# Kernel tuning notes

Measured on AMD Instinct MI355X. Metric: run time of the kernel, lower is better.

Reference implementation:

```python
import jax, jax.numpy as jnp
import numpy as np

B, N, E, FIN, H, D = 256, 1024, 8192, 8, 4, 5
HD = H * D            # GATv2: 4 heads * 5 dim, concat -> 20
OBS = N               # flattened obs length
AOUT = 64             # action_space_output_dim (aggregator output)
HID = 256             # hidden_size
NOUT = 64             # num_outputs (logits)
NEG = 0.2             # GATv2 leaky_relu negative slope
EPS = 1e-5            # batchnorm eps


def setup_inputs() -> dict:
    key = jax.random.key(0)
    ks = jax.random.split(key, 16)
    def lin(k, i, o):
        return (jax.random.normal(k, (i, o), jnp.float32) / np.sqrt(i)).astype(jnp.float32)
    return {
        "x": jax.random.normal(ks[0], (B, N, FIN), jnp.float32),
        "obs": jax.random.normal(ks[1], (B, OBS), jnp.float32),
        "edge_index": jax.random.randint(ks[2], (2, E), 0, N),
        # GATv2 layer 0 (in=FIN) and layer 1 (in=HD)
        "Wl0": lin(ks[3], FIN, HD), "Wr0": lin(ks[4], FIN, HD),
        "att0": (jax.random.normal(ks[5], (H, D), jnp.float32) * 0.1), "b0": jnp.zeros((HD,), jnp.float32),
        "Wl1": lin(ks[6], HD, HD), "Wr1": lin(ks[7], HD, HD),
        "att1": (jax.random.normal(ks[8], (H, D), jnp.float32) * 0.1), "b1": jnp.zeros((HD,), jnp.float32),
        # BatchNorm params per layer (over feature dim)
        "g0": jnp.ones((HD,), jnp.float32), "be0": jnp.zeros((HD,), jnp.float32),
        "g1": jnp.ones((HD,), jnp.float32), "be1": jnp.zeros((HD,), jnp.float32),
        # aggregator linear (mean pool -> action-space dim)
        "Wagg": lin(ks[9], HD, AOUT), "bagg": jnp.zeros((AOUT,), jnp.float32),
        # logits MLP: cat(agg, obs) -> HID -> HID//2 -> NOUT (tanh activations)
        "W1": lin(ks[10], AOUT + OBS, HID), "bh1": jnp.zeros((HID,), jnp.float32),
        "W2": lin(ks[11], HID, HID // 2), "bh2": jnp.zeros((HID // 2,), jnp.float32),
        "Wout": lin(ks[12], HID // 2, NOUT), "bout": jnp.zeros((NOUT,), jnp.float32),
    }


def _gatv2_single(x, src, dst, Wl, Wr, att, bias):
    # x: [N, Fin]; src/dst: [Es] (with self loops)
    xl = (x @ Wl).reshape(N, H, D)
    xr = (x @ Wr).reshape(N, H, D)
    m = jax.nn.leaky_relu(xl[src] + xr[dst], NEG)        # [Es, H, D]
    e = jnp.einsum('ehd,hd->eh', m, att)                 # [Es, H]
    emax = jax.ops.segment_max(e, dst, num_segments=N)   # every node has a self loop
    p = jnp.exp(e - emax[dst])
    s = jax.ops.segment_sum(p, dst, num_segments=N)
    alpha = p / s[dst]                                   # softmax over incoming edges
    out = jax.ops.segment_sum(alpha[:, :, None] * xl[src], dst, num_segments=N)
    return out.reshape(N, HD) + bias


def _bn(x, g, b):
    # training-mode batchnorm over all (batch, node) positions, per feature
    mu = x.mean(axis=(0, 1))
    var = x.var(axis=(0, 1))
    return (x - mu) * jax.lax.rsqrt(var + EPS) * g + b


def reference(x, obs, edge_index, Wl0, Wr0, att0, b0, Wl1, Wr1, att1, b1,
              g0, be0, g1, be1, Wagg, bagg, W1, bh1, W2, bh2, Wout, bout):
    loops = jnp.arange(N)
    src = jnp.concatenate([edge_index[0], loops])
    dst = jnp.concatenate([edge_index[1], loops])
    layer = lambda xb, Wl, Wr, att, bias: jax.vmap(
        lambda xn: _gatv2_single(xn, src, dst, Wl, Wr, att, bias))(xb)
    h = layer(x, Wl0, Wr0, att0, b0)       # [B, N, HD]
    h = _bn(h, g0, be0)
    h = layer(h, Wl1, Wr1, att1, b1)
    h = _bn(h, g1, be1)
    agg = h.mean(axis=1) @ Wagg + bagg     # mean graph pooling -> [B, AOUT]
    f = jnp.concatenate([agg, obs], axis=1)
    f = jnp.tanh(f @ W1 + bh1)
    f = jnp.tanh(f @ W2 + bh2)
    return f @ Wout + bout                 # logits [B, NOUT]
```

## Files before the change

kernel.cpp:

```cpp
#include <hip/hip_runtime.h>
#include <hip/hip_bf16.h>
#include <math.h>

typedef unsigned short u16;
typedef __attribute__((ext_vector_type(8))) short short8;
typedef __attribute__((ext_vector_type(4))) float floatx4;

constexpr int kN   = 1024;
constexpr int kB   = 256;
constexpr int kE   = 8192;
constexpr int kHD  = 20;
constexpr float kEps = 1e-5f;

static __device__ __forceinline__ float u16_bf16_to_f32(u16 v) {
  return __uint_as_float(((unsigned)v) << 16);
}
static __device__ __forceinline__ void unpack2(unsigned u, float& a, float& b) {
  a = __uint_as_float(u << 16);
  b = __uint_as_float(u & 0xffff0000u);
}
static __device__ __forceinline__ u16 f2bf(float f) {
  __hip_bfloat16 h = __float2bfloat16(f);
  return *reinterpret_cast<u16*>(&h);
}
static __device__ __forceinline__ unsigned pack_bf16(float a, float b) {
  return (unsigned)f2bf(a) | ((unsigned)f2bf(b) << 16);
}

__global__ __launch_bounds__(64) void detect_kernel(const unsigned* __restrict__ x,
                                                    int* __restrict__ flag) {
  unsigned w = x[threadIdx.x];
  unsigned e = (w >> 7) & 0xFFu;
  bool plaus = (e >= 114u && e <= 136u);
  unsigned long long b = __ballot(plaus);
  if (threadIdx.x == 0) *flag = (__popcll(b) >= 32) ? 1 : 0;
}

struct SmallConv {
  const void* src[17];
  float* dst[17];
  int n[17];
};

__global__ __launch_bounds__(256) void small_conv_kernel(SmallConv a, const int* __restrict__ flag) {
  int t = blockIdx.x;
  int n = a.n[t];
  float* d = a.dst[t];
  if (*flag) {
    const u16* s = (const u16*)a.src[t];
    for (int i = threadIdx.x; i < n; i += 256) d[i] = u16_bf16_to_f32(s[i]);
  } else {
    const float* s = (const float*)a.src[t];
    for (int i = threadIdx.x; i < n; i += 256) d[i] = s[i];
  }
}

__global__ __launch_bounds__(256) void convert_x_kernel(const void* __restrict__ src,
                                                        float* __restrict__ x_f,
                                                        const int* __restrict__ flag) {
  int rid = blockIdx.x * 256 + threadIdx.x;
  int b = rid >> 10, n = rid & 1023;
  float v[8];
  if (*flag) {
    uint4 r = *((const uint4*)((const u16*)src + (size_t)rid * 8));
    unpack2(r.x, v[0], v[1]); unpack2(r.y, v[2], v[3]);
    unpack2(r.z, v[4], v[5]); unpack2(r.w, v[6], v[7]);
  } else {
    const float4* s = (const float4*)((const float*)src + (size_t)rid * 8);
    float4 r0 = s[0], r1 = s[1];
    v[0] = r0.x; v[1] = r0.y; v[2] = r0.z; v[3] = r0.w;
    v[4] = r1.x; v[5] = r1.y; v[6] = r1.z; v[7] = r1.w;
  }
  float* d = x_f + ((size_t)n * kB + b) * 8;
  ((float4*)d)[0] = make_float4(v[0], v[1], v[2], v[3]);
  ((float4*)d)[1] = make_float4(v[4], v[5], v[6], v[7]);
}

static __device__ __forceinline__ void repack_one(const void* src, u16* dst, int c, int N, int srcbf) {
  int n = c % N;
  int t2 = c / N;
  int q = t2 & 3, kb = t2 >> 2;
  int k0 = kb * 32 + q * 8;
  u16 w[8];
  if (srcbf) {
    const u16* s = (const u16*)src;
#pragma unroll
    for (int j = 0; j < 8; j++) w[j] = s[(size_t)(k0 + j) * N + n];
  } else {
    const float* s = (const float*)src;
#pragma unroll
    for (int j = 0; j < 8; j++) w[j] = f2bf(s[(size_t)(k0 + j) * N + n]);
  }
  uint4 out;
  out.x = (unsigned)w[0] | ((unsigned)w[1] << 16);
  out.y = (unsigned)w[2] | ((unsigned)w[3] << 16);
  out.z = (unsigned)w[4] | ((unsigned)w[5] << 16);
  out.w = (unsigned)w[6] | ((unsigned)w[7] << 16);
  *((uint4*)(dst + (size_t)c * 8)) = out;
}

__global__ __launch_bounds__(256) void repack_kernel(const void* __restrict__ W1,
                                                     const void* __restrict__ W2,
                                                     const void* __restrict__ Wout,
                                                     u16* __restrict__ W1p,
                                                     u16* __restrict__ W2p,
                                                     u16* __restrict__ Woutp,
                                                     const int* __restrict__ flag) {
  int c = blockIdx.x * 256 + threadIdx.x;
  int srcbf = *flag;
  if (c < 34816) repack_one(W1, W1p, c, 256, srcbf);
  else if (c < 34816 + 4096) repack_one(W2, W2p, c - 34816, 128, srcbf);
  else if (c < 34816 + 4096 + 1024) repack_one(Wout, Woutp, c - 34816 - 4096, 64, srcbf);
}

__global__ __launch_bounds__(1024) void build_csr_kernel(const int* __restrict__ ei,
                                                         int* __restrict__ csr_off,
                                                         int* __restrict__ csr_src) {
  __shared__ int cnt[kN];
  __shared__ int tmp[kN];
  __shared__ int cur[kN];
  int t = threadIdx.x;
  cnt[t] = 0;
  __syncthreads();
  for (int e = t; e < kE; e += 1024) atomicAdd(&cnt[ei[kE + e]], 1);
  __syncthreads();
  int deg = cnt[t] + 1;
  tmp[t] = deg;
  __syncthreads();
  for (int o = 1; o < kN; o <<= 1) {
    int add = (t >= o) ? tmp[t - o] : 0;
    __syncthreads();
    tmp[t] += add;
    __syncthreads();
  }
  int excl = tmp[t] - deg;
  csr_off[t] = excl;
  cur[t] = excl;
  if (t == kN - 1) csr_off[kN] = tmp[t];
  __syncthreads();
  for (int e = t; e < kE; e += 1024) {
    int s = ei[e], d2 = ei[kE + e];
    int pos = atomicAdd(&cur[d2], 1);
    csr_src[pos] = s;
  }
  int pos = atomicAdd(&cur[t], 1);
  csr_src[pos] = t;
}

__global__ __launch_bounds__(256) void lin0_kernel(const float* __restrict__ x,
                                                   const float* __restrict__ Wl,
                                                   const float* __restrict__ Wr,
                                                   u16* __restrict__ xlb,
                                                   u16* __restrict__ xrb) {
  __shared__ float wl[8 * kHD], wr[8 * kHD];
  int t = threadIdx.x;
  if (t < 8 * kHD) { wl[t] = Wl[t]; wr[t] = Wr[t]; }
  __syncthreads();
  int n = blockIdx.x, b = t;
  const float4* xp = (const float4*)(x + ((size_t)n * kB + b) * 8);
  float xi[8];
  {
    float4 v0 = xp[0], v1 = xp[1];
    xi[0] = v0.x; xi[1] = v0.y; xi[2] = v0.z; xi[3] = v0.w;
    xi[4] = v1.x; xi[5] = v1.y; xi[6] = v1.z; xi[7] = v1.w;
  }
  float ol[kHD], orr[kHD];
#pragma unroll
  for (int f = 0; f < kHD; f++) {
    float al = 0.f, ar = 0.f;
#pragma unroll
    for (int i = 0; i < 8; i++) {
      al = fmaf(xi[i], wl[i * kHD + f], al);
      ar = fmaf(xi[i], wr[i * kHD + f], ar);
    }
    ol[f] = al; orr[f] = ar;
  }
  uint2* pl = (uint2*)(xlb + ((size_t)n * kB + b) * kHD);
  uint2* pr = (uint2*)(xrb + ((size_t)n * kB + b) * kHD);
#pragma unroll
  for (int k = 0; k < 5; k++) {
    pl[k] = make_uint2(pack_bf16(ol[4 * k], ol[4 * k + 1]), pack_bf16(ol[4 * k + 2], ol[4 * k + 3]));
    pr[k] = make_uint2(pack_bf16(orr[4 * k], orr[4 * k + 1]), pack_bf16(orr[4 * k + 2], orr[4 * k + 3]));
  }
}

__global__ __launch_bounds__(256) void lin1_kernel(const u16* __restrict__ hb,
                                                   const float* __restrict__ Wlp,
                                                   const float* __restrict__ Wrp,
                                                   const float* __restrict__ blp,
                                                   const float* __restrict__ brp,
                                                   u16* __restrict__ xlb,
                                                   u16* __restrict__ xrb) {
  __shared__ float wl[kHD * kHD], wr[kHD * kHD], sbl[kHD], sbr[kHD];
  int t = threadIdx.x;
  for (int idx = t; idx < kHD * kHD; idx += 256) { wl[idx] = Wlp[idx]; wr[idx] = Wrp[idx]; }
  if (t < kHD) { sbl[t] = blp[t]; sbr[t] = brp[t]; }
  __syncthreads();
  int n = blockIdx.x, b = t;
  float hv[kHD];
  {
    const uint2* p = (const uint2*)(hb + ((size_t)n * kB + b) * kHD);
#pragma unroll
    for (int k = 0; k < 5; k++) {
      uint2 v = p[k];
      unpack2(v.x, hv[4 * k], hv[4 * k + 1]);
      unpack2(v.y, hv[4 * k + 2], hv[4 * k + 3]);
    }
  }
  float ol[kHD], orr[kHD];
#pragma unroll
  for (int j = 0; j < kHD; j++) {
    float al = sbl[j], ar = sbr[j];
#pragma unroll
    for (int f = 0; f < kHD; f++) {
      al = fmaf(hv[f], wl[f * kHD + j], al);
      ar = fmaf(hv[f], wr[f * kHD + j], ar);
    }
    ol[j] = al; orr[j] = ar;
  }
  uint2* pl = (uint2*)(xlb + ((size_t)n * kB + b) * kHD);
  uint2* pr = (uint2*)(xrb + ((size_t)n * kB + b) * kHD);
#pragma unroll
  for (int k = 0; k < 5; k++) {
    pl[k] = make_uint2(pack_bf16(ol[4 * k], ol[4 * k + 1]), pack_bf16(ol[4 * k + 2], ol[4 * k + 3]));
    pr[k] = make_uint2(pack_bf16(orr[4 * k], orr[4 * k + 1]), pack_bf16(orr[4 * k + 2], orr[4 * k + 3]));
  }
}

__global__ __launch_bounds__(128) void attn_kernel(const u16* __restrict__ xlb,
                                                   const u16* __restrict__ xrb,
                                                   const int* __restrict__ csr_off,
                                                   const int* __restrict__ csr_src,
                                                   const float* __restrict__ att,
                                                   const float* __restrict__ bias,
                                                   u16* __restrict__ hout,
                                                   float* __restrict__ sums) {
  __shared__ float satt[kHD], sbias[kHD];
  __shared__ float red[2][2 * kHD];
  int t = threadIdx.x;
  if (t < kHD) { satt[t] = att[t]; sbias[t] = bias[t]; }
  __syncthreads();
  int n = blockIdx.x >> 1;
  int b = ((blockIdx.x & 1) << 7) | t;

  float xrv[kHD];
  {
    const uint2* p = (const uint2*)(xrb + ((size_t)n * kB + b) * kHD);
#pragma unroll
    for (int k = 0; k < 5; k++) {
      uint2 v = p[k];
      unpack2(v.x, xrv[4 * k], xrv[4 * k + 1]);
      unpack2(v.y, xrv[4 * k + 2], xrv[4 * k + 3]);
    }
  }
  float s[4] = {0.f, 0.f, 0.f, 0.f};
  float acc[kHD];
#pragma unroll
  for (int f = 0; f < kHD; f++) acc[f] = 0.f;

  int beg = csr_off[n], end = csr_off[n + 1];
  uint2 r[5];
  {
    const uint2* p = (const uint2*)(xlb + ((size_t)csr_src[beg] * kB + b) * kHD);
#pragma unroll
    for (int k = 0; k < 5; k++) r[k] = p[k];
  }
  for (int idx = beg; idx < end; idx++) {
    float xs[kHD];
#pragma unroll
    for (int k = 0; k < 5; k++) {
      unpack2(r[k].x, xs[4 * k], xs[4 * k + 1]);
      unpack2(r[k].y, xs[4 * k + 2], xs[4 * k + 3]);
    }
    if (idx + 1 < end) {
      const uint2* p = (const uint2*)(xlb + ((size_t)csr_src[idx + 1] * kB + b) * kHD);
#pragma unroll
      for (int k = 0; k < 5; k++) r[k] = p[k];
    }
#pragma unroll
    for (int hh = 0; hh < 4; hh++) {
      float e = 0.f;
#pragma unroll
      for (int d = 0; d < 5; d++) {
        int f = hh * 5 + d;
        float v = xs[f] + xrv[f];
        v = fmaxf(v, 0.2f * v);
        e = fmaf(v, satt[f], e);
      }
      float p = __expf(e);
      s[hh] += p;
#pragma unroll
      for (int d = 0; d < 5; d++) {
        int f = hh * 5 + d;
        acc[f] = fmaf(p, xs[f], acc[f]);
      }
    }
  }
  float hv[kHD];
#pragma unroll
  for (int hh = 0; hh < 4; hh++) {
    float inv = 1.f / s[hh];
#pragma unroll
    for (int d = 0; d < 5; d++) {
      int f = hh * 5 + d;
      hv[f] = fmaf(acc[f], inv, sbias[f]);
    }
  }
  {
    uint2* ph = (uint2*)(hout + ((size_t)n * kB + b) * kHD);
#pragma unroll
    for (int k = 0; k < 5; k++)
      ph[k] = make_uint2(pack_bf16(hv[4 * k], hv[4 * k + 1]), pack_bf16(hv[4 * k + 2], hv[4 * k + 3]));
  }
  int lane = t & 63, wv = t >> 6;
#pragma unroll
  for (int f = 0; f < kHD; f++) {
    float a = hv[f], q = hv[f] * hv[f];
    for (int o = 32; o > 0; o >>= 1) { a += __shfl_down(a, o); q += __shfl_down(q, o); }
    if (lane == 0) { red[wv][f] = a; red[wv][kHD + f] = q; }
  }
  __syncthreads();
  if (t < 2 * kHD) atomicAdd(&sums[(blockIdx.x & 7) * 2 * kHD + t], red[0][t] + red[1][t]);
}

__global__ __launch_bounds__(256) void fold_kernel(const float* __restrict__ sums,
                                                   const float* __restrict__ g,
                                                   const float* __restrict__ be,
                                                   const float* __restrict__ Wl1,
                                                   const float* __restrict__ Wr1,
                                                   float* __restrict__ Wlp, float* __restrict__ Wrp,
                                                   float* __restrict__ blp, float* __restrict__ brp) {
  __shared__ float a[kHD], c[kHD];
  __shared__ float tot[2 * kHD];
  int t = threadIdx.x;
  if (t < 2 * kHD) {
    float v = 0.f;
    for (int k = 0; k < 8; k++) v += sums[k * 2 * kHD + t];
    tot[t] = v;
  }
  __syncthreads();
  if (t < kHD) {
    const float inv = 1.0f / (float)(kN * kB);
    float mu = tot[t] * inv;
    float var = tot[kHD + t] * inv - mu * mu;
    float av = g[t] * rsqrtf(var + kEps);
    a[t] = av;
    c[t] = be[t] - mu * av;
  }
  __syncthreads();
  for (int idx = t; idx < kHD * kHD; idx += 256) {
    int f = idx / kHD;
    Wlp[idx] = a[f] * Wl1[idx];
    Wrp[idx] = a[f] * Wr1[idx];
  }
  if (t < kHD) {
    float sl = 0.f, sr = 0.f;
    for (int f = 0; f < kHD; f++) {
      sl += c[f] * Wl1[f * kHD + t];
      sr += c[f] * Wr1[f * kHD + t];
    }
    blp[t] = sl;
    brp[t] = sr;
  }
}

__global__ __launch_bounds__(256) void pool_fin_kernel(const u16* __restrict__ hb,
                                                       const float* __restrict__ sums,
                                                       const float* __restrict__ g1,
                                                       const float* __restrict__ be1,
                                                       const float* __restrict__ Wagg,
                                                       const float* __restrict__ bagg,
                                                       const void* __restrict__ obsraw,
                                                       const int* __restrict__ flag,
                                                       u16* __restrict__ finb) {
  int b = blockIdx.x, t = threadIdx.x;
  float acc[kHD];
#pragma unroll
  for (int f = 0; f < kHD; f++) acc[f] = 0.f;
  for (int n = t; n < kN; n += 256) {
    const uint2* p = (const uint2*)(hb + ((size_t)n * kB + b) * kHD);
#pragma unroll
    for (int k = 0; k < 5; k++) {
      uint2 v = p[k];
      float a0, a1, a2, a3;
      unpack2(v.x, a0, a1); unpack2(v.y, a2, a3);
      acc[4 * k] += a0; acc[4 * k + 1] += a1; acc[4 * k + 2] += a2; acc[4 * k + 3] += a3;
    }
  }
  __shared__ float red[4][kHD];
  __shared__ float tot[2 * kHD], pv[kHD];
#pragma unroll
  for (int f = 0; f < kHD; f++) {
    float v = acc[f];
    for (int o = 32; o > 0; o >>= 1) v += __shfl_down(v, o);
    if ((t & 63) == 0) red[t >> 6][f] = v;
  }
  if (t < 2 * kHD) {
    float v = 0.f;
    for (int k = 0; k < 8; k++) v += sums[k * 2 * kHD + t];
    tot[t] = v;
  }
  __syncthreads();
  if (t < kHD) {
    const float inv = 1.0f / (float)(kN * kB);
    float mu = tot[t] * inv;
    float var = tot[kHD + t] * inv - mu * mu;
    float a1 = g1[t] * rsqrtf(var + kEps);
    float c1 = be1[t] - mu * a1;
    float pool = (red[0][t] + red[1][t] + red[2][t] + red[3][t]) * (1.0f / kN);
    pv[t] = pool * a1 + c1;
  }
  __syncthreads();
  if (t < 64) {
    float agg = bagg[t];
#pragma unroll
    for (int f = 0; f < kHD; f++) agg = fmaf(pv[f], Wagg[f * 64 + t], agg);
    finb[(size_t)b * 1088 + t] = f2bf(agg);
  }
  if (t < 128) {
    uint4* dst = (uint4*)(finb + (size_t)b * 1088 + 64 + t * 8);
    if (*flag) {
      *dst = *((const uint4*)((const u16*)obsraw + (size_t)b * 1024 + t * 8));
    } else {
      const float4* s = (const float4*)((const float*)obsraw + (size_t)b * 1024 + t * 8);
      float4 r0 = s[0], r1 = s[1];
      uint4 o;
      o.x = pack_bf16(r0.x, r0.y); o.y = pack_bf16(r0.z, r0.w);
      o.z = pack_bf16(r1.x, r1.y); o.w = pack_bf16(r1.z, r1.w);
      *dst = o;
    }
  }
}

__global__ __launch_bounds__(256) void mlp1_kernel(const u16* __restrict__ finb,
                                                   const u16* __restrict__ W1p,
                                                   const float* __restrict__ bh1,
                                                   u16* __restrict__ h1b) {
  int tid = threadIdx.x;
  int wave = tid >> 6, lane = tid & 63;
  int tile = blockIdx.x * 4 + wave;
  int m0 = (tile >> 4) << 4, n0 = (tile & 15) << 4;
  int lo = lane & 15, quad = lane >> 4;
  floatx4 acc = {0.f, 0.f, 0.f, 0.f};
  const u16* ap = finb + (size_t)(m0 + lo) * 1088 + quad * 8;
  const u16* bp = W1p + ((size_t)quad * 256 + n0 + lo) * 8;
  for (int kb = 0; kb < 34; kb++) {
    short8 a = *(const short8*)ap; ap += 32;
    short8 bfr = *(const short8*)bp; bp += 4 * 256 * 8;
    acc = __builtin_amdgcn_mfma_f32_16x16x32_bf16(a, bfr, acc, 0, 0, 0);
  }
  float bias = bh1[n0 + lo];
  u16* op = h1b + (size_t)(m0 + quad * 4) * 256 + n0 + lo;
#pragma unroll
  for (int r = 0; r < 4; r++) op[r * 256] = f2bf(tanhf(acc[r] + bias));
}

__global__ __launch_bounds__(256) void mlp23_kernel(const u16* __restrict__ h1b,
                                                    const u16* __restrict__ W2p,
                                                    const u16* __restrict__ Woutp,
                                                    const float* __restrict__ bh2,
                                                    const float* __restrict__ bout,
                                                    const int* __restrict__ flag,
                                                    void* __restrict__ outv) {
  __shared__ __align__(16) u16 h2s[16][128];
  int tid = threadIdx.x;
  int wave = tid >> 6, lane = tid & 63;
  int lo = lane & 15, quad = lane >> 4;
  int m0 = blockIdx.x * 16;
#pragma unroll
  for (int i = 0; i < 2; i++) {
    int n0 = (wave * 2 + i) * 16;
    floatx4 acc = {0.f, 0.f, 0.f, 0.f};
    const u16* ap = h1b + (size_t)(m0 + lo) * 256 + quad * 8;
    const u16* bp = W2p + ((size_t)quad * 128 + n0 + lo) * 8;
    for (int kb = 0; kb < 8; kb++) {
      short8 a = *(const short8*)ap; ap += 32;
      short8 bfr = *(const short8*)bp; bp += 4 * 128 * 8;
      acc = __builtin_amdgcn_mfma_f32_16x16x32_bf16(a, bfr, acc, 0, 0, 0);
    }
    float bias = bh2[n0 + lo];
#pragma unroll
    for (int r = 0; r < 4; r++) h2s[quad * 4 + r][n0 + lo] = f2bf(tanhf(acc[r] + bias));
  }
  __syncthreads();
  {
    int n0 = wave * 16;
    floatx4 acc = {0.f, 0.f, 0.f, 0.f};
    const u16* bp = Woutp + ((size_t)quad * 64 + n0 + lo) * 8;
    for (int kb = 0; kb < 4; kb++) {
      short8 a = *(const short8*)(&h2s[lo][kb * 32 + quad * 8]);
      short8 bfr = *(const short8*)bp; bp += 4 * 64 * 8;
      acc = __builtin_amdgcn_mfma_f32_16x16x32_bf16(a, bfr, acc, 0, 0, 0);
    }
    float bias = bout[n0 + lo];
    if (*flag) {
      __hip_bfloat16* o = (__hip_bfloat16*)outv;
#pragma unroll
      for (int r = 0; r < 4; r++)
        o[(size_t)(m0 + quad * 4 + r) * 64 + n0 + lo] = __float2bfloat16(acc[r] + bias);
    } else {
      float* o = (float*)outv;
#pragma unroll
      for (int r = 0; r < 4; r++)
        o[(size_t)(m0 + quad * 4 + r) * 64 + n0 + lo] = acc[r] + bias;
    }
  }
}

extern "C" void kernel_launch(void* const* d_in, const int* in_sizes, int n_in,
                              void* d_out, int out_size, void* d_ws, size_t ws_size,
                              hipStream_t stream) {
  const int* ei = (const int*)d_in[2];
  char* ws = (char*)d_ws;

  float* sums0   = (float*)(ws + 0);
  float* sums1   = (float*)(ws + 1280);
  int*   flag    = (int*)(ws + 2560);
  int*   csr_off = (int*)(ws + 2816);
  int*   csr_src = (int*)(ws + 7168);
  float* Wlp     = (float*)(ws + 44288);
  float* Wrp     = (float*)(ws + 45888);
  float* blp     = (float*)(ws + 47488);
  float* brp     = (float*)(ws + 47568);
  float* convf   = (float*)(ws + 47872);
  u16*   W1p     = (u16*)(ws + 60416);
  u16*   W2p     = (u16*)(ws + 617472);
  u16*   Woutp   = (u16*)(ws + 683008);
  u16*   finb    = (u16*)(ws + 699392);
  u16*   h1b     = (u16*)(ws + 1256448);
  float* x_f     = (float*)(ws + 1387520);
  u16*   xlb     = (u16*)(ws + 9776128);
  u16*   xrb     = (u16*)(ws + 20261888);
  u16*   hb      = (u16*)(ws + 30747648);

  const int s_din[17] = {3, 4, 5, 6, 7, 8, 9, 10, 11, 12, 13, 14, 15, 16, 18, 20, 22};
  const int s_n[17]   = {160, 160, 20, 20, 400, 400, 20, 20, 20, 20, 20, 20, 1280, 64, 256, 128, 64};
  SmallConv sc;
  float* fptr[17];
  {
    size_t co = 0;
    for (int i = 0; i < 17; i++) {
      sc.src[i] = d_in[s_din[i]];
      sc.dst[i] = convf + co;
      sc.n[i] = s_n[i];
      fptr[i] = convf + co;
      co += (size_t)s_n[i];
    }
  }
  float* Wl0_f = fptr[0],  *Wr0_f = fptr[1],  *att0_f = fptr[2], *b0_f = fptr[3];
  float* Wl1_f = fptr[4],  *Wr1_f = fptr[5],  *att1_f = fptr[6], *b1_f = fptr[7];
  float* g0_f = fptr[8],   *be0_f = fptr[9],  *g1_f = fptr[10],  *be1_f = fptr[11];
  float* Wagg_f = fptr[12], *bagg_f = fptr[13], *bh1_f = fptr[14], *bh2_f = fptr[15];
  float* bout_f = fptr[16];

  hipMemsetAsync(ws, 0, 2560, stream);
  detect_kernel<<<1, 64, 0, stream>>>((const unsigned*)d_in[0], flag);
  small_conv_kernel<<<17, 256, 0, stream>>>(sc, flag);
  convert_x_kernel<<<1024, 256, 0, stream>>>(d_in[0], x_f, flag);
  repack_kernel<<<156, 256, 0, stream>>>(d_in[17], d_in[19], d_in[21], W1p, W2p, Woutp, flag);
  build_csr_kernel<<<1, 1024, 0, stream>>>(ei, csr_off, csr_src);

  lin0_kernel<<<kN, 256, 0, stream>>>(x_f, Wl0_f, Wr0_f, xlb, xrb);
  attn_kernel<<<2 * kN, 128, 0, stream>>>(xlb, xrb, csr_off, csr_src, att0_f, b0_f, hb, sums0);
  fold_kernel<<<1, 256, 0, stream>>>(sums0, g0_f, be0_f, Wl1_f, Wr1_f, Wlp, Wrp, blp, brp);
  lin1_kernel<<<kN, 256, 0, stream>>>(hb, Wlp, Wrp, blp, brp, xlb, xrb);
  attn_kernel<<<2 * kN, 128, 0, stream>>>(xlb, xrb, csr_off, csr_src, att1_f, b1_f, hb, sums1);
  pool_fin_kernel<<<kB, 256, 0, stream>>>(hb, sums1, g1_f, be1_f, Wagg_f, bagg_f,
                                          d_in[1], flag, finb);
  mlp1_kernel<<<64, 256, 0, stream>>>(finb, W1p, bh1_f, h1b);
  mlp23_kernel<<<16, 256, 0, stream>>>(h1b, W2p, Woutp, bh2_f, bout_f, flag, d_out);
}
```

Measured before the change: 234.5 us.

## Fuse setup kernels and fold BN into lin1, reducing launch count

Merges the memset, dtype detection, small-parameter conversion, x conversion, weight repack, CSR build and layer-0 linear into one multi-role setup kernel. The x transpose now happens inside lin0, so the fp32 staging buffer goes away. The BatchNorm fold is merged into lin1, and every kernel recomputes the dtype flag and converts its parameters inline instead of reading pre-converted copies. The aim is to remove about seven launches and an extra pass over x. The cost is redundant per-block flag detection and parameter conversion, plus a serial CSR block that now shares its launch with heavy work.

```diff
diff --git a/kernel.cpp b/kernel.cpp
--- a/kernel.cpp
+++ b/kernel.cpp
@@ -27,56 +27,20 @@
   return (unsigned)f2bf(a) | ((unsigned)f2bf(b) << 16);
 }
 
-__global__ __launch_bounds__(64) void detect_kernel(const unsigned* __restrict__ x,
-                                                    int* __restrict__ flag) {
-  unsigned w = x[threadIdx.x];
+static __device__ __forceinline__ int detect_flag(const unsigned* __restrict__ x) {
+  unsigned w = x[threadIdx.x & 63];
   unsigned e = (w >> 7) & 0xFFu;
   bool plaus = (e >= 114u && e <= 136u);
   unsigned long long b = __ballot(plaus);
-  if (threadIdx.x == 0) *flag = (__popcll(b) >= 32) ? 1 : 0;
-}
-
-struct SmallConv {
-  const void* src[17];
-  float* dst[17];
-  int n[17];
-};
-
-__global__ __launch_bounds__(256) void small_conv_kernel(SmallConv a, const int* __restrict__ flag) {
-  int t = blockIdx.x;
-  int n = a.n[t];
-  float* d = a.dst[t];
-  if (*flag) {
-    const u16* s = (const u16*)a.src[t];
-    for (int i = threadIdx.x; i < n; i += 256) d[i] = u16_bf16_to_f32(s[i]);
-  } else {
-    const float* s = (const float*)a.src[t];
-    for (int i = threadIdx.x; i < n; i += 256) d[i] = s[i];
-  }
-}
-
-__global__ __launch_bounds__(256) void convert_x_kernel(const void* __restrict__ src,
-                                                        float* __restrict__ x_f,
-                                                        const int* __restrict__ flag) {
-  int rid = blockIdx.x * 256 + threadIdx.x;
-  int b = rid >> 10, n = rid & 1023;
-  float v[8];
-  if (*flag) {
-    uint4 r = *((const uint4*)((const u16*)src + (size_t)rid * 8));
-    unpack2(r.x, v[0], v[1]); unpack2(r.y, v[2], v[3]);
-    unpack2(r.z, v[4], v[5]); unpack2(r.w, v[6], v[7]);
-  } else {
-    const float4* s = (const float4*)((const float*)src + (size_t)rid * 8);
-    float4 r0 = s[0], r1 = s[1];
-    v[0] = r0.x; v[1] = r0.y; v[2] = r0.z; v[3] = r0.w;
-    v[4] = r1.x; v[5] = r1.y; v[6] = r1.z; v[7] = r1.w;
-  }
-  float* d = x_f + ((size_t)n * kB + b) * 8;
-  ((float4*)d)[0] = make_float4(v[0], v[1], v[2], v[3]);
-  ((float4*)d)[1] = make_float4(v[4], v[5], v[6], v[7]);
-}
-
-static __device__ __forceinline__ void repack_one(const void* src, u16* dst, int c, int N, int srcbf) {
+  return (__popcll(b) >= 32) ? 1 : 0;
+}
+static __device__ __forceinline__ float ldconv(const void* __restrict__ p, int i, int flag) {
+  return flag ? u16_bf16_to_f32(((const u16*)p)[i]) : ((const float*)p)[i];
+}
+
+static __device__ __forceinline__ void repack_one(const void* __restrict__ src,
+                                                  u16* __restrict__ dst,
+                                                  int c, int N, int srcbf) {
   int n = c % N;
   int t2 = c / N;
   int q = t2 & 3, kb = t2 >> 2;
@@ -99,131 +63,89 @@
   *((uint4*)(dst + (size_t)c * 8)) = out;
 }
 
-__global__ __launch_bounds__(256) void repack_kernel(const void* __restrict__ W1,
-                                                     const void* __restrict__ W2,
-                                                     const void* __restrict__ Wout,
-                                                     u16* __restrict__ W1p,
-                                                     u16* __restrict__ W2p,
-                                                     u16* __restrict__ Woutp,
-                                                     const int* __restrict__ flag) {
-  int c = blockIdx.x * 256 + threadIdx.x;
-  int srcbf = *flag;
-  if (c < 34816) repack_one(W1, W1p, c, 256, srcbf);
-  else if (c < 34816 + 4096) repack_one(W2, W2p, c - 34816, 128, srcbf);
-  else if (c < 34816 + 4096 + 1024) repack_one(Wout, Woutp, c - 34816 - 4096, 64, srcbf);
-}
-
-__global__ __launch_bounds__(1024) void build_csr_kernel(const int* __restrict__ ei,
-                                                         int* __restrict__ csr_off,
-                                                         int* __restrict__ csr_src) {
-  __shared__ int cnt[kN];
-  __shared__ int tmp[kN];
-  __shared__ int cur[kN];
+__global__ __launch_bounds__(1024) void setup_kernel(
+    const unsigned* __restrict__ xdet,
+    const void* __restrict__ xin,
+    const int* __restrict__ ei,
+    const void* __restrict__ Wl0, const void* __restrict__ Wr0,
+    const void* __restrict__ W1, const void* __restrict__ W2, const void* __restrict__ Wout,
+    int* __restrict__ csr_off, int* __restrict__ csr_src,
+    float* __restrict__ sums,
+    u16* __restrict__ W1p, u16* __restrict__ W2p, u16* __restrict__ Woutp,
+    u16* __restrict__ xlb, u16* __restrict__ xrb) {
+  int bid = blockIdx.x;
   int t = threadIdx.x;
-  cnt[t] = 0;
-  __syncthreads();
-  for (int e = t; e < kE; e += 1024) atomicAdd(&cnt[ei[kE + e]], 1);
-  __syncthreads();
-  int deg = cnt[t] + 1;
-  tmp[t] = deg;
-  __syncthreads();
-  for (int o = 1; o < kN; o <<= 1) {
-    int add = (t >= o) ? tmp[t - o] : 0;
+  if (bid == 0) {
+    __shared__ int cnt[kN];
+    __shared__ int tmp[kN];
+    __shared__ int cur[kN];
+    cnt[t] = 0;
     __syncthreads();
-    tmp[t] += add;
+    for (int e = t; e < kE; e += 1024) atomicAdd(&cnt[ei[kE + e]], 1);
     __syncthreads();
-  }
-  int excl = tmp[t] - deg;
-  csr_off[t] = excl;
-  cur[t] = excl;
-  if (t == kN - 1) csr_off[kN] = tmp[t];
-  __syncthreads();
-  for (int e = t; e < kE; e += 1024) {
-    int s = ei[e], d2 = ei[kE + e];
-    int pos = atomicAdd(&cur[d2], 1);
-    csr_src[pos] = s;
-  }
-  int pos = atomicAdd(&cur[t], 1);
-  csr_src[pos] = t;
-}
-
-__global__ __launch_bounds__(256) void lin0_kernel(const float* __restrict__ x,
-                                                   const float* __restrict__ Wl,
-                                                   const float* __restrict__ Wr,
-                                                   u16* __restrict__ xlb,
-                                                   u16* __restrict__ xrb) {
-  __shared__ float wl[8 * kHD], wr[8 * kHD];
-  int t = threadIdx.x;
-  if (t < 8 * kHD) { wl[t] = Wl[t]; wr[t] = Wr[t]; }
-  __syncthreads();
-  int n = blockIdx.x, b = t;
-  const float4* xp = (const float4*)(x + ((size_t)n * kB + b) * 8);
-  float xi[8];
-  {
-    float4 v0 = xp[0], v1 = xp[1];
-    xi[0] = v0.x; xi[1] = v0.y; xi[2] = v0.z; xi[3] = v0.w;
-    xi[4] = v1.x; xi[5] = v1.y; xi[6] = v1.z; xi[7] = v1.w;
-  }
-  float ol[kHD], orr[kHD];
-#pragma unroll
-  for (int f = 0; f < kHD; f++) {
-    float al = 0.f, ar = 0.f;
-#pragma unroll
-    for (int i = 0; i < 8; i++) {
-      al = fmaf(xi[i], wl[i * kHD + f], al);
-      ar = fmaf(xi[i], wr[i * kHD + f], ar);
-    }
-    ol[f] = al; orr[f] = ar;
-  }
-  uint2* pl = (uint2*)(xlb + ((size_t)n * kB + b) * kHD);
-  uint2* pr = (uint2*)(xrb + ((size_t)n * kB + b) * kHD);
-#pragma unroll
-  for (int k = 0; k < 5; k++) {
-    pl[k] = make_uint2(pack_bf16(ol[4 * k], ol[4 * k + 1]), pack_bf16(ol[4 * k + 2], ol[4 * k + 3]));
-    pr[k] = make_uint2(pack_bf16(orr[4 * k], orr[4 * k + 1]), pack_bf16(orr[4 * k + 2], orr[4 * k + 3]));
-  }
-}
-
-__global__ __launch_bounds__(256) void lin1_kernel(const u16* __restrict__ hb,
-                                                   const float* __restrict__ Wlp,
-                                                   const float* __restrict__ Wrp,
-                                                   const float* __restrict__ blp,
-                                                   const float* __restrict__ brp,
-                                                   u16* __restrict__ xlb,
-                                                   u16* __restrict__ xrb) {
-  __shared__ float wl[kHD * kHD], wr[kHD * kHD], sbl[kHD], sbr[kHD];
-  int t = threadIdx.x;
-  for (int idx = t; idx < kHD * kHD; idx += 256) { wl[idx] = Wlp[idx]; wr[idx] = Wrp[idx]; }
-  if (t < kHD) { sbl[t] = blp[t]; sbr[t] = brp[t]; }
-  __syncthreads();
-  int n = blockIdx.x, b = t;
-  float hv[kHD];
-  {
-    const uint2* p = (const uint2*)(hb + ((size_t)n * kB + b) * kHD);
+    int deg = cnt[t] + 1;
+    tmp[t] = deg;
+    __syncthreads();
+    for (int o = 1; o < kN; o <<= 1) {
+      int add = (t >= o) ? tmp[t - o] : 0;
+      __syncthreads();
+      tmp[t] += add;
+      __syncthreads();
+    }
+    int excl = tmp[t] - deg;
+    csr_off[t] = excl;
+    cur[t] = excl;
+    if (t == kN - 1) csr_off[kN] = tmp[t];
+    __syncthreads();
+    for (int e = t; e < kE; e += 1024) {
+      int s = ei[e], d2 = ei[kE + e];
+      int pos = atomicAdd(&cur[d2], 1);
+      csr_src[pos] = s;
+    }
+    int pos = atomicAdd(&cur[t], 1);
+    csr_src[pos] = t;
+    if (t < 640) sums[t] = 0.f;
+  } else if (bid <= 39) {
+    int flag = detect_flag(xdet);
+    int c = (bid - 1) * 1024 + t;
+    if (c < 34816) repack_one(W1, W1p, c, 256, flag);
+    else if (c < 38912) repack_one(W2, W2p, c - 34816, 128, flag);
+    else repack_one(Wout, Woutp, c - 38912, 64, flag);
+  } else {
+    int flag = detect_flag(xdet);
+    __shared__ float wl[8 * kHD], wr[8 * kHD];
+    if (t < 8 * kHD) { wl[t] = ldconv(Wl0, t, flag); wr[t] = ldconv(Wr0, t, flag); }
+    __syncthreads();
+    int n = (bid - 40) * 4 + (t >> 8), b = t & 255;
+    float xi[8];
+    if (flag) {
+      uint4 r = *((const uint4*)((const u16*)xin + ((size_t)b * kN + n) * 8));
+      unpack2(r.x, xi[0], xi[1]); unpack2(r.y, xi[2], xi[3]);
+      unpack2(r.z, xi[4], xi[5]); unpack2(r.w, xi[6], xi[7]);
+    } else {
+      const float4* s = (const float4*)((const float*)xin + ((size_t)b * kN + n) * 8);
+      float4 v0 = s[0], v1 = s[1];
+      xi[0] = v0.x; xi[1] = v0.y; xi[2] = v0.z; xi[3] = v0.w;
+      xi[4] = v1.x; xi[5] = v1.y; xi[6] = v1.z; xi[7] = v1.w;
+    }
+    float ol[kHD], orr[kHD];
+#pragma unroll
+    for (int f = 0; f < kHD; f++) {
+      float al = 0.f, ar = 0.f;
+#pragma unroll
+      for (int i = 0; i < 8; i++) {
+        al = fmaf(xi[i], wl[i * kHD + f], al);
+        ar = fmaf(xi[i], wr[i * kHD + f], ar);
+      }
+      ol[f] = al; orr[f] = ar;
+    }
+    uint2* pl = (uint2*)(xlb + ((size_t)n * kB + b) * kHD);
+    uint2* pr = (uint2*)(xrb + ((size_t)n * kB + b) * kHD);
 #pragma unroll
     for (int k = 0; k < 5; k++) {
-      uint2 v = p[k];
-      unpack2(v.x, hv[4 * k], hv[4 * k + 1]);
-      unpack2(v.y, hv[4 * k + 2], hv[4 * k + 3]);
-    }
-  }
-  float ol[kHD], orr[kHD];
-#pragma unroll
-  for (int j = 0; j < kHD; j++) {
-    float al = sbl[j], ar = sbr[j];
-#pragma unroll
-    for (int f = 0; f < kHD; f++) {
-      al = fmaf(hv[f], wl[f * kHD + j], al);
-      ar = fmaf(hv[f], wr[f * kHD + j], ar);
-    }
-    ol[j] = al; orr[j] = ar;
-  }
-  uint2* pl = (uint2*)(xlb + ((size_t)n * kB + b) * kHD);
-  uint2* pr = (uint2*)(xrb + ((size_t)n * kB + b) * kHD);
-#pragma unroll
-  for (int k = 0; k < 5; k++) {
-    pl[k] = make_uint2(pack_bf16(ol[4 * k], ol[4 * k + 1]), pack_bf16(ol[4 * k + 2], ol[4 * k + 3]));
-    pr[k] = make_uint2(pack_bf16(orr[4 * k], orr[4 * k + 1]), pack_bf16(orr[4 * k + 2], orr[4 * k + 3]));
+      pl[k] = make_uint2(pack_bf16(ol[4 * k], ol[4 * k + 1]), pack_bf16(ol[4 * k + 2], ol[4 * k + 3]));
+      pr[k] = make_uint2(pack_bf16(orr[4 * k], orr[4 * k + 1]), pack_bf16(orr[4 * k + 2], orr[4 * k + 3]));
+    }
   }
 }
 
@@ -231,14 +153,16 @@
                                                    const u16* __restrict__ xrb,
                                                    const int* __restrict__ csr_off,
                                                    const int* __restrict__ csr_src,
-                                                   const float* __restrict__ att,
-                                                   const float* __restrict__ bias,
+                                                   const void* __restrict__ attraw,
+                                                   const void* __restrict__ braw,
+                                                   const unsigned* __restrict__ xdet,
                                                    u16* __restrict__ hout,
                                                    float* __restrict__ sums) {
   __shared__ float satt[kHD], sbias[kHD];
   __shared__ float red[2][2 * kHD];
+  int flag = detect_flag(xdet);
   int t = threadIdx.x;
-  if (t < kHD) { satt[t] = att[t]; sbias[t] = bias[t]; }
+  if (t < kHD) { satt[t] = ldconv(attraw, t, flag); sbias[t] = ldconv(braw, t, flag); }
   __syncthreads();
   int n = blockIdx.x >> 1;
   int b = ((blockIdx.x & 1) << 7) | t;
@@ -323,19 +247,22 @@
   if (t < 2 * kHD) atomicAdd(&sums[(blockIdx.x & 7) * 2 * kHD + t], red[0][t] + red[1][t]);
 }
 
-__global__ __launch_bounds__(256) void fold_kernel(const float* __restrict__ sums,
-                                                   const float* __restrict__ g,
-                                                   const float* __restrict__ be,
-                                                   const float* __restrict__ Wl1,
-                                                   const float* __restrict__ Wr1,
-                                                   float* __restrict__ Wlp, float* __restrict__ Wrp,
-                                                   float* __restrict__ blp, float* __restrict__ brp) {
-  __shared__ float a[kHD], c[kHD];
-  __shared__ float tot[2 * kHD];
+__global__ __launch_bounds__(256) void lin1_kernel(const u16* __restrict__ hb,
+                                                   const float* __restrict__ sums0,
+                                                   const void* __restrict__ g0,
+                                                   const void* __restrict__ be0,
+                                                   const void* __restrict__ Wl1,
+                                                   const void* __restrict__ Wr1,
+                                                   const unsigned* __restrict__ xdet,
+                                                   u16* __restrict__ xlb,
+                                                   u16* __restrict__ xrb) {
+  __shared__ float wl[kHD * kHD], wr[kHD * kHD], sbl[kHD], sbr[kHD];
+  __shared__ float sa[kHD], sc[kHD], tot[2 * kHD];
+  int flag = detect_flag(xdet);
   int t = threadIdx.x;
   if (t < 2 * kHD) {
     float v = 0.f;
-    for (int k = 0; k < 8; k++) v += sums[k * 2 * kHD + t];
+    for (int k = 0; k < 8; k++) v += sums0[k * 2 * kHD + t];
     tot[t] = v;
   }
   __syncthreads();
@@ -343,36 +270,67 @@
     const float inv = 1.0f / (float)(kN * kB);
     float mu = tot[t] * inv;
     float var = tot[kHD + t] * inv - mu * mu;
-    float av = g[t] * rsqrtf(var + kEps);
-    a[t] = av;
-    c[t] = be[t] - mu * av;
+    float av = ldconv(g0, t, flag) * rsqrtf(var + kEps);
+    sa[t] = av;
+    sc[t] = ldconv(be0, t, flag) - mu * av;
   }
   __syncthreads();
   for (int idx = t; idx < kHD * kHD; idx += 256) {
     int f = idx / kHD;
-    Wlp[idx] = a[f] * Wl1[idx];
-    Wrp[idx] = a[f] * Wr1[idx];
+    wl[idx] = sa[f] * ldconv(Wl1, idx, flag);
+    wr[idx] = sa[f] * ldconv(Wr1, idx, flag);
   }
   if (t < kHD) {
     float sl = 0.f, sr = 0.f;
     for (int f = 0; f < kHD; f++) {
-      sl += c[f] * Wl1[f * kHD + t];
-      sr += c[f] * Wr1[f * kHD + t];
-    }
-    blp[t] = sl;
-    brp[t] = sr;
+      sl += sc[f] * ldconv(Wl1, f * kHD + t, flag);
+      sr += sc[f] * ldconv(Wr1, f * kHD + t, flag);
+    }
+    sbl[t] = sl;
+    sbr[t] = sr;
+  }
+  __syncthreads();
+  int n = blockIdx.x, b = t;
+  float hv[kHD];
+  {
+    const uint2* p = (const uint2*)(hb + ((size_t)n * kB + b) * kHD);
+#pragma unroll
+    for (int k = 0; k < 5; k++) {
+      uint2 v = p[k];
+      unpack2(v.x, hv[4 * k], hv[4 * k + 1]);
+      unpack2(v.y, hv[4 * k + 2], hv[4 * k + 3]);
+    }
+  }
+  float ol[kHD], orr[kHD];
+#pragma unroll
+  for (int j = 0; j < kHD; j++) {
+    float al = sbl[j], ar = sbr[j];
+#pragma unroll
+    for (int f = 0; f < kHD; f++) {
+      al = fmaf(hv[f], wl[f * kHD + j], al);
+      ar = fmaf(hv[f], wr[f * kHD + j], ar);
+    }
+    ol[j] = al; orr[j] = ar;
+  }
+  uint2* pl = (uint2*)(xlb + ((size_t)n * kB + b) * kHD);
+  uint2* pr = (uint2*)(xrb + ((size_t)n * kB + b) * kHD);
+#pragma unroll
+  for (int k = 0; k < 5; k++) {
+    pl[k] = make_uint2(pack_bf16(ol[4 * k], ol[4 * k + 1]), pack_bf16(ol[4 * k + 2], ol[4 * k + 3]));
+    pr[k] = make_uint2(pack_bf16(orr[4 * k], orr[4 * k + 1]), pack_bf16(orr[4 * k + 2], orr[4 * k + 3]));
   }
 }
 
 __global__ __launch_bounds__(256) void pool_fin_kernel(const u16* __restrict__ hb,
-                                                       const float* __restrict__ sums,
-                                                       const float* __restrict__ g1,
-                                                       const float* __restrict__ be1,
-                                                       const float* __restrict__ Wagg,
-                                                       const float* __restrict__ bagg,
+                                                       const float* __restrict__ sums1,
+                                                       const void* __restrict__ g1,
+                                                       const void* __restrict__ be1,
+                                                       const void* __restrict__ Wagg,
+                                                       const void* __restrict__ bagg,
                                                        const void* __restrict__ obsraw,
-                                                       const int* __restrict__ flag,
+                                                       const unsigned* __restrict__ xdet,
                                                        u16* __restrict__ finb) {
+  int flag = detect_flag(xdet);
   int b = blockIdx.x, t = threadIdx.x;
   float acc[kHD];
 #pragma unroll
@@ -397,7 +355,7 @@
   }
   if (t < 2 * kHD) {
     float v = 0.f;
-    for (int k = 0; k < 8; k++) v += sums[k * 2 * kHD + t];
+    for (int k = 0; k < 8; k++) v += sums1[k * 2 * kHD + t];
     tot[t] = v;
   }
   __syncthreads();
@@ -405,21 +363,21 @@
     const float inv = 1.0f / (float)(kN * kB);
     float mu = tot[t] * inv;
     float var = tot[kHD + t] * inv - mu * mu;
-    float a1 = g1[t] * rsqrtf(var + kEps);
-    float c1 = be1[t] - mu * a1;
+    float a1 = ldconv(g1, t, flag) * rsqrtf(var + kEps);
+    float c1 = ldconv(be1, t, flag) - mu * a1;
     float pool = (red[0][t] + red[1][t] + red[2][t] + red[3][t]) * (1.0f / kN);
     pv[t] = pool * a1 + c1;
   }
   __syncthreads();
   if (t < 64) {
-    float agg = bagg[t];
-#pragma unroll
-    for (int f = 0; f < kHD; f++) agg = fmaf(pv[f], Wagg[f * 64 + t], agg);
+    float agg = ldconv(bagg, t, flag);
+#pragma unroll
+    for (int f = 0; f < kHD; f++) agg = fmaf(pv[f], ldconv(Wagg, f * 64 + t, flag), agg);
     finb[(size_t)b * 1088 + t] = f2bf(agg);
   }
   if (t < 128) {
     uint4* dst = (uint4*)(finb + (size_t)b * 1088 + 64 + t * 8);
-    if (*flag) {
+    if (flag) {
       *dst = *((const uint4*)((const u16*)obsraw + (size_t)b * 1024 + t * 8));
     } else {
       const float4* s = (const float4*)((const float*)obsraw + (size_t)b * 1024 + t * 8);
@@ -434,8 +392,10 @@
 
 __global__ __launch_bounds__(256) void mlp1_kernel(const u16* __restrict__ finb,
                                                    const u16* __restrict__ W1p,
-                                                   const float* __restrict__ bh1,
+                                                   const void* __restrict__ bh1,
+                                                   const unsigned* __restrict__ xdet,
                                                    u16* __restrict__ h1b) {
+  int flag = detect_flag(xdet);
   int tid = threadIdx.x;
   int wave = tid >> 6, lane = tid & 63;
   int tile = blockIdx.x * 4 + wave;
@@ -449,7 +409,7 @@
     short8 bfr = *(const short8*)bp; bp += 4 * 256 * 8;
     acc = __builtin_amdgcn_mfma_f32_16x16x32_bf16(a, bfr, acc, 0, 0, 0);
   }
-  float bias = bh1[n0 + lo];
+  float bias = ldconv(bh1, n0 + lo, flag);
   u16* op = h1b + (size_t)(m0 + quad * 4) * 256 + n0 + lo;
 #pragma unroll
   for (int r = 0; r < 4; r++) op[r * 256] = f2bf(tanhf(acc[r] + bias));
@@ -458,11 +418,12 @@
 __global__ __launch_bounds__(256) void mlp23_kernel(const u16* __restrict__ h1b,
                                                     const u16* __restrict__ W2p,
                                                     const u16* __restrict__ Woutp,
-                                                    const float* __restrict__ bh2,
-                                                    const float* __restrict__ bout,
-                                                    const int* __restrict__ flag,
+                                                    const void* __restrict__ bh2,
+                                                    const void* __restrict__ bout,
+                                                    const unsigned* __restrict__ xdet,
                                                     void* __restrict__ outv) {
   __shared__ __align__(16) u16 h2s[16][128];
+  int flag = detect_flag(xdet);
   int tid = threadIdx.x;
   int wave = tid >> 6, lane = tid & 63;
   int lo = lane & 15, quad = lane >> 4;
@@ -478,7 +439,7 @@
       short8 bfr = *(const short8*)bp; bp += 4 * 128 * 8;
       acc = __builtin_amdgcn_mfma_f32_16x16x32_bf16(a, bfr, acc, 0, 0, 0);
     }
-    float bias = bh2[n0 + lo];
+    float bias = ldconv(bh2, n0 + lo, flag);
 #pragma unroll
     for (int r = 0; r < 4; r++) h2s[quad * 4 + r][n0 + lo] = f2bf(tanhf(acc[r] + bias));
   }
@@ -492,8 +453,8 @@
       short8 bfr = *(const short8*)bp; bp += 4 * 64 * 8;
       acc = __builtin_amdgcn_mfma_f32_16x16x32_bf16(a, bfr, acc, 0, 0, 0);
     }
-    float bias = bout[n0 + lo];
-    if (*flag) {
+    float bias = ldconv(bout, n0 + lo, flag);
+    if (flag) {
       __hip_bfloat16* o = (__hip_bfloat16*)outv;
 #pragma unroll
       for (int r = 0; r < 4; r++)
@@ -510,63 +471,37 @@
 extern "C" void kernel_launch(void* const* d_in, const int* in_sizes, int n_in,
                               void* d_out, int out_size, void* d_ws, size_t ws_size,
                               hipStream_t stream) {
+  char* ws = (char*)d_ws;
+  float* sums    = (float*)(ws + 0);
+  float* sums0   = sums;
+  float* sums1   = sums + 320;
+  int*   csr_off = (int*)(ws + 2560);
+  int*   csr_src = (int*)(ws + 6912);
+  u16*   W1p     = (u16*)(ws + 44032);
+  u16*   W2p     = (u16*)(ws + 601088);
+  u16*   Woutp   = (u16*)(ws + 666624);
+  u16*   h1b     = (u16*)(ws + 683008);
+  u16*   finb    = (u16*)(ws + 814080);
+  u16*   xlb     = (u16*)(ws + 1371136);
+  u16*   xrb     = (u16*)(ws + 11856896);
+  u16*   hb      = (u16*)(ws + 22342656);
+
+  const unsigned* xdet = (const unsigned*)d_in[0];
   const int* ei = (const int*)d_in[2];
-  char* ws = (char*)d_ws;
-
-  float* sums0   = (float*)(ws + 0);
-  float* sums1   = (float*)(ws + 1280);
-  int*   flag    = (int*)(ws + 2560);
-  int*   csr_off = (int*)(ws + 2816);
-  int*   csr_src = (int*)(ws + 7168);
-  float* Wlp     = (float*)(ws + 44288);
-  float* Wrp     = (float*)(ws + 45888);
-  float* blp     = (float*)(ws + 47488);
-  float* brp     = (float*)(ws + 47568);
-  float* convf   = (float*)(ws + 47872);
-  u16*   W1p     = (u16*)(ws + 60416);
-  u16*   W2p     = (u16*)(ws + 617472);
-  u16*   Woutp   = (u16*)(ws + 683008);
-  u16*   finb    = (u16*)(ws + 699392);
-  u16*   h1b     = (u16*)(ws + 1256448);
-  float* x_f     = (float*)(ws + 1387520);
-  u16*   xlb     = (u16*)(ws + 9776128);
-  u16*   xrb     = (u16*)(ws + 20261888);
-  u16*   hb      = (u16*)(ws + 30747648);
-
-  const int s_din[17] = {3, 4, 5, 6, 7, 8, 9, 10, 11, 12, 13, 14, 15, 16, 18, 20, 22};
-  const int s_n[17]   = {160, 160, 20, 20, 400, 400, 20, 20, 20, 20, 20, 20, 1280, 64, 256, 128, 64};
-  SmallConv sc;
-  float* fptr[17];
-  {
-    size_t co = 0;
-    for (int i = 0; i < 17; i++) {
-      sc.src[i] = d_in[s_din[i]];
-      sc.dst[i] = convf + co;
-      sc.n[i] = s_n[i];
-      fptr[i] = convf + co;
-      co += (size_t)s_n[i];
-    }
-  }
-  float* Wl0_f = fptr[0],  *Wr0_f = fptr[1],  *att0_f = fptr[2], *b0_f = fptr[3];
-  float* Wl1_f = fptr[4],  *Wr1_f = fptr[5],  *att1_f = fptr[6], *b1_f = fptr[7];
-  float* g0_f = fptr[8],   *be0_f = fptr[9],  *g1_f = fptr[10],  *be1_f = fptr[11];
-  float* Wagg_f = fptr[12], *bagg_f = fptr[13], *bh1_f = fptr[14], *bh2_f = fptr[15];
-  float* bout_f = fptr[16];
-
-  hipMemsetAsync(ws, 0, 2560, stream);
-  detect_kernel<<<1, 64, 0, stream>>>((const unsigned*)d_in[0], flag);
-  small_conv_kernel<<<17, 256, 0, stream>>>(sc, flag);
-  convert_x_kernel<<<1024, 256, 0, stream>>>(d_in[0], x_f, flag);
-  repack_kernel<<<156, 256, 0, stream>>>(d_in[17], d_in[19], d_in[21], W1p, W2p, Woutp, flag);
-  build_csr_kernel<<<1, 1024, 0, stream>>>(ei, csr_off, csr_src);
-
-  lin0_kernel<<<kN, 256, 0, stream>>>(x_f, Wl0_f, Wr0_f, xlb, xrb);
-  attn_kernel<<<2 * kN, 128, 0, stream>>>(xlb, xrb, csr_off, csr_src, att0_f, b0_f, hb, sums0);
-  fold_kernel<<<1, 256, 0, stream>>>(sums0, g0_f, be0_f, Wl1_f, Wr1_f, Wlp, Wrp, blp, brp);
-  lin1_kernel<<<kN, 256, 0, stream>>>(hb, Wlp, Wrp, blp, brp, xlb, xrb);
-  attn_kernel<<<2 * kN, 128, 0, stream>>>(xlb, xrb, csr_off, csr_src, att1_f, b1_f, hb, sums1);
-  pool_fin_kernel<<<kB, 256, 0, stream>>>(hb, sums1, g1_f, be1_f, Wagg_f, bagg_f,
-                                          d_in[1], flag, finb);
-  mlp1_kernel<<<64, 256, 0, stream>>>(finb, W1p, bh1_f, h1b);
-  mlp23_kernel<<<16, 256, 0, stream>>>(h1b, W2p, Woutp, bh2_f, bout_f, flag, d_out);
-}
+
+  setup_kernel<<<296, 1024, 0, stream>>>(xdet, d_in[0], ei,
+                                         d_in[3], d_in[4],
+                                         d_in[17], d_in[19], d_in[21],
+                                         csr_off, csr_src, sums,
+                                         W1p, W2p, Woutp, xlb, xrb);
+  attn_kernel<<<2 * kN, 128, 0, stream>>>(xlb, xrb, csr_off, csr_src,
+                                          d_in[5], d_in[6], xdet, hb, sums0);
+  lin1_kernel<<<kN, 256, 0, stream>>>(hb, sums0, d_in[11], d_in[12],
+                                      d_in[7], d_in[8], xdet, xlb, xrb);
+  attn_kernel<<<2 * kN, 128, 0, stream>>>(xlb, xrb, csr_off, csr_src,
+                                          d_in[9], d_in[10], xdet, hb, sums1);
+  pool_fin_kernel<<<kB, 256, 0, stream>>>(hb, sums1, d_in[13], d_in[14],
+                                          d_in[15], d_in[16], d_in[1], xdet, finb);
+  mlp1_kernel<<<64, 256, 0, stream>>>(finb, W1p, d_in[18], xdet, h1b);
+  mlp23_kernel<<<16, 256, 0, stream>>>(h1b, W2p, Woutp, d_in[20], d_in[22], xdet, d_out);
+}
```

New measurement: 214.4 us. 8.6% less time.
